# Performance work log

Measured on AMD Instinct MI355X. Metric: run time of the kernel, lower is better.

The kernel has to match this reference:

```python
import jax, jax.numpy as jnp
import numpy as np

# ---- static config (eval-mode RPN, torchvision-style FPN) ----
LEVEL_HW = [(200, 200), (100, 100), (50, 50), (25, 25), (13, 13)]
STRIDES = [4, 8, 16, 32, 64]
SIZES = [32, 64, 128, 256, 512]
A = 3                      # anchors per location (3 aspect ratios)
IMG_H, IMG_W = 800, 800
PRE_N, POST_N = 1000, 1000 # pre/post NMS top-n (testing)
NMS_TH, SCORE_TH, MIN_SIZE = 0.7, 0.0, 1e-3
BBOX_CLIP = 4.135166556742356  # log(1000/16), BoxCoder clamp
NUM_PER_LEVEL = [A * h * w for h, w in LEVEL_HW]


def _make_anchors():
    ratios = np.array([0.5, 1.0, 2.0])
    hr = np.sqrt(ratios)
    wr = 1.0 / hr
    out = []
    for (H, W), size, stride in zip(LEVEL_HW, SIZES, STRIDES):
        ws, hs = wr * size, hr * size
        base = np.stack([-ws / 2, -hs / 2, ws / 2, hs / 2], axis=1)  # [A,4]
        sx = np.arange(W) * stride
        sy = np.arange(H) * stride
        yy, xx = np.meshgrid(sy, sx, indexing='ij')
        shifts = np.stack([xx.ravel(), yy.ravel(), xx.ravel(), yy.ravel()], axis=1)
        out.append((shifts[:, None, :] + base[None, :, :]).reshape(-1, 4))
    return np.concatenate(out, 0).astype(np.float32)


def setup_inputs() -> dict:
    key = jax.random.key(0)
    ks = jax.random.split(key, 10)
    N = 4
    inp = {}
    for i, (h, w) in enumerate(LEVEL_HW):
        inp[f'obj{i}'] = jax.random.normal(ks[i], (N, A, h, w), jnp.float32)
        inp[f'delta{i}'] = 0.5 * jax.random.normal(ks[5 + i], (N, 4 * A, h, w), jnp.float32)
    inp['anchors'] = jnp.asarray(_make_anchors())
    return inp


def _decode(deltas, anchors):
    # BoxCoder.decode with weights (1,1,1,1)
    wa = anchors[:, 2] - anchors[:, 0]
    ha = anchors[:, 3] - anchors[:, 1]
    cxa = anchors[:, 0] + 0.5 * wa
    cya = anchors[:, 1] + 0.5 * ha
    dx, dy = deltas[..., 0], deltas[..., 1]
    dw = jnp.minimum(deltas[..., 2], BBOX_CLIP)
    dh = jnp.minimum(deltas[..., 3], BBOX_CLIP)
    cx = dx * wa + cxa
    cy = dy * ha + cya
    w = jnp.exp(dw) * wa
    h = jnp.exp(dh) * ha
    return jnp.stack([cx - 0.5 * w, cy - 0.5 * h, cx + 0.5 * w, cy + 0.5 * h], -1)


def _box_iou(b1, b2):
    a1 = (b1[:, 2] - b1[:, 0]) * (b1[:, 3] - b1[:, 1])
    a2 = (b2[:, 2] - b2[:, 0]) * (b2[:, 3] - b2[:, 1])
    lt = jnp.maximum(b1[:, None, :2], b2[None, :, :2])
    rb = jnp.minimum(b1[:, None, 2:], b2[None, :, 2:])
    wh = jnp.clip(rb - lt, 0.0)
    inter = wh[..., 0] * wh[..., 1]
    return inter / (a1[:, None] + a2[None, :] - inter)


def _nms_keep(iou, valid):
    # greedy NMS over score-sorted boxes; valid marks surviving pre-filters
    K = iou.shape[0]
    def body(sup, i):
        k = valid[i] & jnp.logical_not(sup[i])
        sup = sup | (k & (iou[i] > NMS_TH))
        return sup, k
    _, keeps = jax.lax.scan(body, jnp.zeros(K, bool), jnp.arange(K))
    return keeps


def _per_image(boxes, scores, lvl):
    # clip_boxes_to_image
    x1 = jnp.clip(boxes[:, 0], 0.0, IMG_W)
    y1 = jnp.clip(boxes[:, 1], 0.0, IMG_H)
    x2 = jnp.clip(boxes[:, 2], 0.0, IMG_W)
    y2 = jnp.clip(boxes[:, 3], 0.0, IMG_H)
    boxes = jnp.stack([x1, y1, x2, y2], -1)
    # remove_small_boxes + score_thresh as validity mask
    valid = (x2 - x1 >= MIN_SIZE) & (y2 - y1 >= MIN_SIZE) & (scores >= SCORE_TH)
    ms = jnp.where(valid, scores, -1.0)
    order = jnp.argsort(-ms)
    b_s, v_s, s_s, l_s = boxes[order], valid[order], scores[order], lvl[order]
    # batched_nms trick: offset boxes by level so levels never overlap
    bn = jax.lax.stop_gradient(b_s) + (l_s.astype(boxes.dtype) * (IMG_W + 1.0))[:, None]
    keep = _nms_keep(_box_iou(bn, bn), v_s)
    sel_key = jnp.where(keep, jax.lax.stop_gradient(s_s), -1.0)
    topv, topi = jax.lax.top_k(sel_key, POST_N)
    m = topv > -0.5
    fb = jnp.where(m[:, None], b_s[topi], 0.0)
    fs = jnp.where(m, s_s[topi], 0.0)
    return fb, fs


def reference(obj0, obj1, obj2, obj3, obj4, delta0, delta1, delta2, delta3, delta4, anchors):
    objs = [obj0, obj1, obj2, obj3, obj4]
    dels = [delta0, delta1, delta2, delta3, delta4]
    N = obj0.shape[0]
    # permute_and_flatten + concat (objectness C=1)
    obj = jnp.concatenate([o.transpose(0, 2, 3, 1).reshape(N, -1) for o in objs], 1)
    dl = jnp.concatenate([
        d.reshape(N, A, 4, d.shape[2], d.shape[3]).transpose(0, 3, 4, 1, 2).reshape(N, -1, 4)
        for d in dels], 1)
    proposals = _decode(dl, anchors)  # [N, total, 4]
    levels = jnp.concatenate([jnp.full((n,), i, jnp.int32) for i, n in enumerate(NUM_PER_LEVEL)])
    # per-level top-k (static split)
    idxs, off = [], 0
    for n in NUM_PER_LEVEL:
        k = min(PRE_N, n)
        _, ti = jax.lax.top_k(obj[:, off:off + n], k)
        idxs.append(ti + off)
        off += n
    top_idx = jnp.concatenate(idxs, 1)  # [N, K]
    sel_obj = jnp.take_along_axis(obj, top_idx, 1)
    sel_lvl = levels[top_idx]
    sel_box = jnp.take_along_axis(proposals, top_idx[..., None], 1)
    scores = jax.nn.sigmoid(sel_obj)
    fb, fs = jax.vmap(_per_image)(sel_box, scores, sel_lvl)
    return fb, fs
```

## Files before the change

### kernel.cpp

```cpp
#include <hip/hip_runtime.h>
#include <cstdint>
#include <cstddef>

#define NLV 5
#define NIMG 4
#define NSEL 4507
#define TSEL (NIMG * NSEL)
#define POSTN 1000
#define TCAP 8192
#define TTCAP 2048
#define NHB 16
#define PBLK 64
#define PCH 1875

__device__ const int d_W[NLV]    = {200, 100, 50, 25, 13};
__device__ const int d_NL[NLV]   = {120000, 30000, 7500, 1875, 507};
__device__ const int d_KOFF[6]   = {0, 120000, 150000, 157500, 159375, 159882};
__device__ const int d_LOFF[6]   = {0, 1000, 2000, 3000, 4000, 4507};
__device__ const int d_KL[NLV]   = {1000, 1000, 1000, 1000, 507};

struct Ptrs {
    const float* obj[NLV];
    const float* del[NLV];
    const float* anch;
};

__device__ inline unsigned int dkey_of(float f) {
    unsigned int u = __float_as_uint(f);
    unsigned int mk = (u & 0x80000000u) ? ~u : (u | 0x80000000u);
    return ~mk;
}
__device__ inline float logit_from_dkey(unsigned int dk) {
    unsigned int mk = ~dk;
    unsigned int u = (mk & 0x80000000u) ? (mk & 0x7fffffffu) : ~mk;
    return __uint_as_float(u);
}

__global__ __launch_bounds__(256) void k_hist(Ptrs P, unsigned int* hist) {
    int l = blockIdx.y, n = blockIdx.z;
    int nl_sz = d_NL[l];
    if (d_KL[l] >= nl_sz) return;
    int nlid = n * NLV + l;
    __shared__ unsigned int h[2048];
    for (int i = threadIdx.x; i < 2048; i += 256) h[i] = 0;
    __syncthreads();
    const float* ob = P.obj[l] + (size_t)n * nl_sz;
    int chunk = (nl_sz + NHB - 1) / NHB;
    int beg = blockIdx.x * chunk;
    int end = min(beg + chunk, nl_sz);
    for (int t = beg + (int)threadIdx.x; t < end; t += 256)
        atomicAdd(&h[dkey_of(ob[t]) >> 21], 1u);
    __syncthreads();
    unsigned int* out = hist + ((size_t)nlid * NHB + blockIdx.x) * 2048;
    for (int i = threadIdx.x; i < 2048; i += 256) out[i] = h[i];
}

__global__ __launch_bounds__(1024) void k_thresh(const unsigned int* hist,
                                                 unsigned int* thr,
                                                 int* scnt, int* tcnt) {
    int nlid = blockIdx.x;
    int l = nlid % NLV;
    if (threadIdx.x == 0) { scnt[nlid] = 0; tcnt[nlid] = 0; }
    if (d_KL[l] >= d_NL[l]) return;
    int tid = threadIdx.x, w = tid >> 6, lane = tid & 63;
    __shared__ unsigned int wpre[16];
    const unsigned int* hb = hist + (size_t)nlid * NHB * 2048;
    unsigned int v0 = 0, v1 = 0;
    #pragma unroll
    for (int sh = 0; sh < NHB; ++sh) {
        v0 += hb[sh * 2048 + 2 * tid];
        v1 += hb[sh * 2048 + 2 * tid + 1];
    }
    unsigned int s = v0 + v1;
    unsigned int ps = s;
    #pragma unroll
    for (int d = 1; d < 64; d <<= 1) {
        unsigned int t2 = (unsigned int)__shfl_up((int)ps, d, 64);
        if (lane >= d) ps += t2;
    }
    if (lane == 63) wpre[w] = ps;
    __syncthreads();
    unsigned int base = 0;
    #pragma unroll
    for (int ww = 0; ww < 16; ++ww) if (ww < w) base += wpre[ww];
    unsigned int incl = base + ps;
    unsigned int target = (unsigned int)d_KL[l];
    unsigned int exc0 = incl - s, inc0 = incl - v1;
    unsigned int exc1 = inc0,    inc1 = incl;
    if (exc0 < target && target <= inc0) { thr[nlid * 2] = 2 * tid;     thr[nlid * 2 + 1] = exc0; }
    if (exc1 < target && target <= inc1) { thr[nlid * 2] = 2 * tid + 1; thr[nlid * 2 + 1] = exc1; }
}

__global__ __launch_bounds__(256) void k_pick(Ptrs P, const unsigned int* thr,
                                              int* scnt, int* tcnt,
                                              int* cg, float* cl,
                                              unsigned long long* tiebuf) {
    int l = blockIdx.y, n = blockIdx.z;
    int nl_sz = d_NL[l], kl = d_KL[l];
    int nlid = n * NLV + l;
    const float* ob = P.obj[l] + (size_t)n * nl_sz;
    int cbase = n * NSEL + d_LOFF[l];
    int koff = d_KOFF[l];
    int Wl = d_W[l], HW = Wl * Wl;
    int chunk = (nl_sz + PBLK - 1) / PBLK;
    int beg = blockIdx.x * chunk;
    int end = min(beg + chunk, nl_sz);
    int tid = threadIdx.x;

    if (kl >= nl_sz) {
        for (int t = beg + tid; t < end; t += 256) {
            int a = t / HW, rem = t - a * HW;
            int p = rem * 3 + a;
            cg[cbase + p] = koff + p;
            cl[cbase + p] = ob[t];
        }
        return;
    }
    __shared__ int sp[PCH];
    __shared__ float sl[PCH];
    __shared__ unsigned long long tb[PCH];
    __shared__ int nsel, ntie, sbase, tbase;
    if (tid == 0) { nsel = 0; ntie = 0; }
    __syncthreads();

    unsigned int b0 = thr[nlid * 2];
    for (int t = beg + tid; t < end; t += 256) {
        float lg = ob[t];
        unsigned int dk = dkey_of(lg);
        unsigned int bin = dk >> 21;
        if (bin < b0) {
            int pos = atomicAdd(&nsel, 1);
            int a = t / HW, rem = t - a * HW;
            sp[pos] = rem * 3 + a;
            sl[pos] = lg;
        } else if (bin == b0) {
            int pos = atomicAdd(&ntie, 1);
            int a = t / HW, rem = t - a * HW;
            tb[pos] = ((unsigned long long)dk << 17) |
                      (unsigned long long)(unsigned int)(rem * 3 + a);
        }
    }
    __syncthreads();
    if (tid == 0) {
        sbase = atomicAdd(&scnt[nlid], nsel);
        tbase = atomicAdd(&tcnt[nlid], ntie);
    }
    __syncthreads();
    int ns = nsel, nt = ntie, sb = sbase, tbs = tbase;
    for (int i = tid; i < ns; i += 256) {
        cg[cbase + sb + i] = koff + sp[i];
        cl[cbase + sb + i] = sl[i];
    }
    for (int i = tid; i < nt; i += 256) {
        int slot = tbs + i;
        if (slot < TCAP) tiebuf[(size_t)nlid * TCAP + slot] = tb[i];
    }
}

__global__ __launch_bounds__(1024) void k_tie(const unsigned int* thr, const int* tcnt,
                                              const unsigned long long* tiebuf,
                                              int* cg, float* cl) {
    int nlid = blockIdx.x;
    int n = nlid / NLV, l = nlid % NLV;
    if (d_KL[l] >= d_NL[l]) return;
    __shared__ unsigned long long kk[TCAP];
    __shared__ unsigned long long tt[TTCAP];
    __shared__ unsigned int h2[2048];
    __shared__ unsigned int wpre[16];
    __shared__ unsigned int s_b1, s_before;
    __shared__ int ctr, ttc;
    int c = min(tcnt[nlid], TCAP);
    unsigned int cnt_lt = thr[nlid * 2 + 1];
    int need = d_KL[l] - (int)cnt_lt;
    int tid = threadIdx.x, w = tid >> 6, lane = tid & 63;
    if (tid == 0) { ctr = 0; ttc = 0; }
    h2[tid] = 0; h2[tid + 1024] = 0;
    for (int i = tid; i < c; i += 1024) kk[i] = tiebuf[(size_t)nlid * TCAP + i];
    __syncthreads();
    for (int i = tid; i < c; i += 1024)
        atomicAdd(&h2[(unsigned int)((kk[i] >> 27) & 0x7ffull)], 1u);
    __syncthreads();
    unsigned int v0 = h2[2 * tid], v1 = h2[2 * tid + 1];
    unsigned int s = v0 + v1, ps = s;
    #pragma unroll
    for (int d = 1; d < 64; d <<= 1) {
        unsigned int t2 = (unsigned int)__shfl_up((int)ps, d, 64);
        if (lane >= d) ps += t2;
    }
    if (lane == 63) wpre[w] = ps;
    __syncthreads();
    unsigned int base = 0;
    #pragma unroll
    for (int ww = 0; ww < 16; ++ww) if (ww < w) base += wpre[ww];
    unsigned int incl = base + ps;
    unsigned int target = (unsigned int)need;
    unsigned int exc0 = incl - s, inc0 = incl - v1;
    unsigned int exc1 = inc0,    inc1 = incl;
    if (exc0 < target && target <= inc0) { s_b1 = 2 * tid;     s_before = exc0; }
    if (exc1 < target && target <= inc1) { s_b1 = 2 * tid + 1; s_before = exc1; }
    __syncthreads();
    unsigned int b1 = s_b1;
    int before = (int)s_before;
    int cbase = n * NSEL + d_LOFF[l];
    int koff = d_KOFF[l];
    for (int i = tid; i < c; i += 1024) {
        unsigned long long ki = kk[i];
        unsigned int sb = (unsigned int)((ki >> 27) & 0x7ffull);
        if (sb < b1) {
            int slot = atomicAdd(&ctr, 1);
            int p = (int)(ki & 0x1ffffull);
            cg[cbase + (int)cnt_lt + slot] = koff + p;
            cl[cbase + (int)cnt_lt + slot] = logit_from_dkey((unsigned int)(ki >> 17));
        } else if (sb == b1) {
            int j = atomicAdd(&ttc, 1);
            if (j < TTCAP) tt[j] = ki;
        }
    }
    __syncthreads();
    int c2 = min(ttc, TTCAP);
    int need2 = need - before;
    for (int i = tid; i < c2; i += 1024) {
        unsigned long long ki = tt[i];
        int rank = 0;
        for (int j = 0; j < c2; ++j) rank += (tt[j] < ki) ? 1 : 0;
        if (rank < need2) {
            int p = (int)(ki & 0x1ffffull);
            cg[cbase + (int)cnt_lt + before + rank] = koff + p;
            cl[cbase + (int)cnt_lt + before + rank] = logit_from_dkey((unsigned int)(ki >> 17));
        }
    }
}

__global__ __launch_bounds__(256) void k_build(Ptrs P, const int* cg, const float* cl,
                                               unsigned long long* pkey,
                                               float4* pbox, float4* pbn, float* plog) {
#pragma clang fp contract(off)
    int t = blockIdx.x * blockDim.x + threadIdx.x;
    if (t >= NIMG * NLV * 1024) return;
    int nl = t >> 10, j = t & 1023;
    int n = nl / NLV, l = nl % NLV;
    if (j >= d_KL[l]) {
        pkey[t] = ((unsigned long long)0xFFFFFFFFu << 27) | (unsigned long long)j;
        pbox[t] = make_float4(0.f, 0.f, 0.f, 0.f);
        pbn[t]  = make_float4(0.f, 0.f, 0.f, 0.f);
        plog[t] = 0.f;
        return;
    }
    int s = n * NSEL + d_LOFF[l] + j;
    int gidx = cg[s];
    float lg = cl[s];
    int p = gidx - d_KOFF[l];
    int Wl = d_W[l];
    int HW = Wl * Wl;
    int a = p % 3, hw = p / 3;
    int h = hw / Wl, w = hw - h * Wl;
    const float* dl = P.del[l];
    size_t base = (size_t)(n * 12 + a * 4) * HW + (size_t)h * Wl + w;
    float dx = dl[base], dy = dl[base + HW];
    float dw = dl[base + 2 * (size_t)HW], dh = dl[base + 3 * (size_t)HW];
    const float* an = P.anch + 4 * (size_t)gidx;
    float ax1 = an[0], ay1 = an[1], ax2 = an[2], ay2 = an[3];
    float wa = ax2 - ax1, ha = ay2 - ay1;
    float cxa = ax1 + 0.5f * wa, cya = ay1 + 0.5f * ha;
    const float CLIPC = (float)4.135166556742356;
    dw = fminf(dw, CLIPC); dh = fminf(dh, CLIPC);
    float cx = dx * wa + cxa;
    float cy = dy * ha + cya;
    float ww = expf(dw) * wa;
    float hh = expf(dh) * ha;
    float x1 = cx - 0.5f * ww, y1 = cy - 0.5f * hh;
    float x2 = cx + 0.5f * ww, y2 = cy + 0.5f * hh;
    x1 = fminf(fmaxf(x1, 0.0f), 800.0f);
    y1 = fminf(fmaxf(y1, 0.0f), 800.0f);
    x2 = fminf(fmaxf(x2, 0.0f), 800.0f);
    y2 = fminf(fmaxf(y2, 0.0f), 800.0f);
    bool valid = (x2 - x1 >= 1e-3f) && (y2 - y1 >= 1e-3f);
    float off = (float)l * 801.0f;
    pbox[t] = make_float4(x1, y1, x2, y2);
    pbn[t]  = make_float4(x1 + off, y1 + off, x2 + off, y2 + off);
    plog[t] = lg;
    unsigned int sk = valid ? dkey_of(lg) : 0xffffffffu;
    pkey[t] = ((unsigned long long)sk << 27) |
              ((unsigned long long)(unsigned int)p << 10) | (unsigned long long)j;
}

__global__ __launch_bounds__(512) void k_sortL(const unsigned long long* pkey,
                                               const float4* pbox, const float4* pbn,
                                               const float* plog,
                                               unsigned long long* skey,
                                               float4* sboxL, float4* cboxL, float* slogL,
                                               int* ccnt) {
    __shared__ unsigned long long s[1024];
    int nl = blockIdx.x, tid = threadIdx.x;
    s[tid] = pkey[nl * 1024 + tid];
    s[tid + 512] = pkey[nl * 1024 + tid + 512];
    __syncthreads();
    for (int k = 2; k <= 1024; k <<= 1) {
        for (int j = k >> 1; j > 0; j >>= 1) {
            int i = ((tid & ~(j - 1)) << 1) | (tid & (j - 1));
            int ix = i | j;
            bool up = ((i & k) == 0);
            unsigned long long A = s[i], B = s[ix];
            if ((A > B) == up) { s[i] = B; s[ix] = A; }
            __syncthreads();
        }
    }
    for (int e = tid; e < 1024; e += 512) {
        unsigned long long key = s[e];
        int j = (int)(key & 0x3ffull);
        int src = nl * 1024 + j;
        skey[nl * 1024 + e] = key;
        sboxL[nl * 1024 + e] = pbox[src];
        cboxL[nl * 1024 + e] = pbn[src];
        slogL[nl * 1024 + e] = plog[src];
        bool v = (key >> 27) != 0xFFFFFFFFull;
        bool vn = (e < 1023) ? ((s[e + 1] >> 27) != 0xFFFFFFFFull) : false;
        if (e == 0 && !v) ccnt[nl] = 0;
        if (v && (e == 1023 || !vn)) ccnt[nl] = e + 1;
    }
}

__global__ __launch_bounds__(256) void k_mask(const float4* cboxL, const int* ccnt,
                                              unsigned long long* MT) {
#pragma clang fp contract(off)
    int n = blockIdx.z, l = blockIdx.y;
    int ci = blockIdx.x >> 4, cj = blockIdx.x & 15;
    int nl = n * NLV + l;
    int cnt = ccnt[nl];
    int nw = (cnt + 63) / 64;
    if (cj < ci || cj >= nw) return;
    __shared__ float4 bi[64], bj[64];
    int tid = threadIdx.x;
    if (tid < 64) bj[tid] = cboxL[nl * 1024 + cj * 64 + tid];
    else if (tid < 128) bi[tid - 64] = cboxL[nl * 1024 + ci * 64 + (tid - 64)];
    __syncthreads();
    int w = tid >> 6, lane = tid & 63;
    float4 B = bj[lane];
    float a2 = (B.z - B.x) * (B.w - B.y);
    unsigned long long* outp = MT + ((size_t)nl * 16 + cj) * 1024 + ci * 64;
    #pragma unroll
    for (int t = 0; t < 16; ++t) {
        int i = w * 16 + t;
        float4 A = bi[i];
        float a1 = (A.z - A.x) * (A.w - A.y);
        float ltx = fmaxf(A.x, B.x), lty = fmaxf(A.y, B.y);
        float rbx = fminf(A.z, B.z), rby = fminf(A.w, B.w);
        float wx = fmaxf(rbx - ltx, 0.f), wy = fmaxf(rby - lty, 0.f);
        float inter = wx * wy;
        float iou = inter / ((a1 + a2) - inter);
        unsigned long long word = __ballot(iou > 0.7f);
        if (lane == 0) outp[i] = word;
    }
}

__global__ __launch_bounds__(1024) void k_scan(const unsigned long long* MT,
                                               const int* ccnt,
                                               unsigned long long* keepL) {
    int l = blockIdx.x, n = blockIdx.y;
    int nl = n * NLV + l;
    int tid = threadIdx.x, w = tid >> 6, lane = tid & 63;
    __shared__ unsigned long long pendS[16];
    __shared__ unsigned long long defS[16];
    int cnt = ccnt[nl];
    int nw = (cnt + 63) / 64;

    const unsigned long long* base = MT + ((size_t)nl * 16 + w) * 1024;
    unsigned long long Dmask = 0;
    if (w < nw)
        Dmask = base[(size_t)w * 64 + lane] & ~((2ull << lane) - 1ull);
    unsigned long long rows[15];
    #pragma unroll
    for (int cc = 0; cc < 15; ++cc)
        rows[cc] = (cc < w && w < nw) ? base[(size_t)cc * 64 + lane] : 0ull;

    int nb = max(0, min(64, cnt - w * 64));
    unsigned long long pend_w = (nb == 64) ? ~0ull : ((nb > 0) ? ((1ull << nb) - 1ull) : 0ull);
    unsigned long long K_w = 0;
    if (lane == 0) pendS[w] = pend_w;
    __syncthreads();

    for (int round = 0; round < 1024; ++round) {
        unsigned long long any = 0;
        #pragma unroll
        for (int cc = 0; cc < 16; ++cc) any |= pendS[cc];
        if (!any) break;
        unsigned long long acc = ((pendS[w] >> lane) & 1ull) ? Dmask : 0ull;
        #pragma unroll
        for (int cc = 0; cc < 15; ++cc)
            if (cc < w) acc |= ((pendS[cc] >> lane) & 1ull) ? rows[cc] : 0ull;
        unsigned int vlo = (unsigned int)acc, vhi = (unsigned int)(acc >> 32);
        #pragma unroll
        for (int m = 1; m < 64; m <<= 1) {
            vlo |= (unsigned int)__shfl_xor((int)vlo, m, 64);
            vhi |= (unsigned int)__shfl_xor((int)vhi, m, 64);
        }
        unsigned long long sup = ((unsigned long long)vhi << 32) | (unsigned long long)vlo;
        unsigned long long def_w = pend_w & ~sup;
        K_w |= def_w;
        if (lane == 0) defS[w] = def_w;
        __syncthreads();
        unsigned long long acc2 = ((defS[w] >> lane) & 1ull) ? Dmask : 0ull;
        #pragma unroll
        for (int cc = 0; cc < 15; ++cc)
            if (cc < w) acc2 |= ((defS[cc] >> lane) & 1ull) ? rows[cc] : 0ull;
        unsigned int rlo = (unsigned int)acc2, rhi = (unsigned int)(acc2 >> 32);
        #pragma unroll
        for (int m = 1; m < 64; m <<= 1) {
            rlo |= (unsigned int)__shfl_xor((int)rlo, m, 64);
            rhi |= (unsigned int)__shfl_xor((int)rhi, m, 64);
        }
        unsigned long long rem = ((unsigned long long)rhi << 32) | (unsigned long long)rlo;
        pend_w &= ~def_w & ~rem;
        if (lane == 0) pendS[w] = pend_w;
        __syncthreads();
    }
    if (lane == 0) keepL[nl * 16 + w] = K_w;
}

__global__ __launch_bounds__(1024) void k_rank(const unsigned long long* skey,
                                               const unsigned long long* keepL,
                                               const int* ccnt,
                                               const float4* sboxL, const float* slogL,
                                               float* out) {
    int n = blockIdx.x, tid = threadIdx.x;
    __shared__ unsigned long long KS[NLV][1024];
    __shared__ unsigned long long kd[NLV][16];
    __shared__ int kpre[NLV][17];
    __shared__ int lcnt[NLV];
    for (int i = tid; i < POSTN; i += 1024) {
        ((float4*)out)[n * POSTN + i] = make_float4(0.f, 0.f, 0.f, 0.f);
        out[NIMG * POSTN * 4 + n * POSTN + i] = 0.f;
    }
    for (int e = tid; e < NLV * 1024; e += 1024)
        ((unsigned long long*)KS)[e] = skey[(size_t)n * NLV * 1024 + e];
    if (tid < NLV * 16) ((unsigned long long*)kd)[tid] = keepL[n * NLV * 16 + tid];
    if (tid < NLV) lcnt[tid] = ccnt[n * NLV + tid];
    __syncthreads();
    if (tid < NLV) {
        int run = 0;
        for (int q = 0; q < 16; ++q) { kpre[tid][q] = run; run += (int)__popcll(kd[tid][q]); }
        kpre[tid][16] = run;
    }
    __syncthreads();
    for (int e = tid; e < NLV * 1024; e += 1024) {
        int l = e >> 10, i = e & 1023;
        if (i >= lcnt[l]) continue;
        int q = i >> 6, b = i & 63;
        if (!((kd[l][q] >> b) & 1ull)) continue;
        int rank = kpre[l][q] + (int)__popcll(kd[l][q] & ((1ull << b) - 1ull));
        unsigned int sk = (unsigned int)(KS[l][i] >> 27);
        for (int l2 = 0; l2 < NLV; ++l2) {
            if (l2 == l) continue;
            int c2 = lcnt[l2];
            unsigned long long bound = (l2 < l)
                ? (((unsigned long long)sk + 1ull) << 27)
                : ((unsigned long long)sk << 27);
            int lo = 0, hi = c2;
            while (lo < hi) {
                int mid = (lo + hi) >> 1;
                if (KS[l2][mid] < bound) lo = mid + 1; else hi = mid;
            }
            int mq = lo >> 6, mb = lo & 63;
            rank += kpre[l2][mq] + (mb ? (int)__popcll(kd[l2][mq] & ((1ull << mb) - 1ull)) : 0);
        }
        if (rank < POSTN) {
            ((float4*)out)[n * POSTN + rank] = sboxL[(size_t)(n * NLV + l) * 1024 + i];
            float lg = slogL[(size_t)(n * NLV + l) * 1024 + i];
            out[NIMG * POSTN * 4 + n * POSTN + rank] = 1.0f / (1.0f + expf(-lg));
        }
    }
}

extern "C" void kernel_launch(void* const* d_in, const int* in_sizes, int n_in,
                              void* d_out, int out_size, void* d_ws, size_t ws_size,
                              hipStream_t stream) {
    Ptrs P;
    bool interleaved = (in_sizes[1] == 4 * in_sizes[0]);
    for (int i = 0; i < NLV; ++i) {
        if (interleaved) {
            P.obj[i] = (const float*)d_in[2 * i];
            P.del[i] = (const float*)d_in[2 * i + 1];
        } else {
            P.obj[i] = (const float*)d_in[i];
            P.del[i] = (const float*)d_in[NLV + i];
        }
    }
    P.anch = (const float*)d_in[10];

    char* w = (char*)d_ws;
    size_t off = 0;
    auto alloc = [&](size_t bytes) {
        void* p = w + off;
        off = (off + bytes + 255) & ~(size_t)255;
        return p;
    };
    const size_t NLT = (size_t)NIMG * NLV * 1024;
    unsigned int* hist = (unsigned int*)alloc((size_t)NIMG * NLV * NHB * 2048 * 4);
    int* scnt = (int*)alloc(256);
    int* tcnt = (int*)alloc(256);
    unsigned int* thr = (unsigned int*)alloc((size_t)NIMG * NLV * 2 * 4);
    unsigned long long* tiebuf = (unsigned long long*)alloc((size_t)NIMG * NLV * TCAP * 8);
    int* cg      = (int*)alloc((size_t)TSEL * 4);
    float* cl    = (float*)alloc((size_t)TSEL * 4);
    unsigned long long* pkey = (unsigned long long*)alloc(NLT * 8);
    float4* pbox = (float4*)alloc(NLT * 16);
    float4* pbn  = (float4*)alloc(NLT * 16);
    float* plog  = (float*)alloc(NLT * 4);
    unsigned long long* skey = (unsigned long long*)alloc(NLT * 8);
    float4* sboxL = (float4*)alloc(NLT * 16);
    float4* cboxL = (float4*)alloc(NLT * 16);
    float* slogL  = (float*)alloc(NLT * 4);
    int* ccnt    = (int*)alloc((size_t)NIMG * NLV * 4);
    unsigned long long* keepL = (unsigned long long*)alloc((size_t)NIMG * NLV * 16 * 8);
    unsigned long long* MT = (unsigned long long*)alloc((size_t)NIMG * NLV * 16 * 1024 * 8);
    (void)ws_size; (void)n_in;

    k_hist<<<dim3(NHB, NLV, NIMG), 256, 0, stream>>>(P, hist);
    k_thresh<<<NIMG * NLV, 1024, 0, stream>>>(hist, thr, scnt, tcnt);
    k_pick<<<dim3(PBLK, NLV, NIMG), 256, 0, stream>>>(P, thr, scnt, tcnt, cg, cl, tiebuf);
    k_tie<<<NIMG * NLV, 1024, 0, stream>>>(thr, tcnt, tiebuf, cg, cl);
    k_build<<<(NIMG * NLV * 1024) / 256, 256, 0, stream>>>(P, cg, cl, pkey, pbox, pbn, plog);
    k_sortL<<<NIMG * NLV, 512, 0, stream>>>(pkey, pbox, pbn, plog, skey, sboxL, cboxL, slogL, ccnt);
    k_mask<<<dim3(256, NLV, NIMG), 256, 0, stream>>>(cboxL, ccnt, MT);
    k_scan<<<dim3(NLV, NIMG), 1024, 0, stream>>>(MT, ccnt, keepL);
    k_rank<<<NIMG, 1024, 0, stream>>>(skey, keepL, ccnt, sboxL, slogL, (float*)d_out);
}
```

Baseline: 169.5 us.

## Fuse threshold, tie-break and box build into neighbouring kernels via last-block pattern

The threshold search now runs in the last-finishing block of k_hist, and the tie resolution now runs in the last-finishing block of k_pick. Both use an atomic arrival counter and thread fences, with the counters zeroed by a small memset. Box decoding moves from k_build into k_sortL, which keeps boxes in shared memory instead of writing and re-reading pbox, pbn, plog and pkey through global memory. This cuts three kernel launches and some global round-trips. In exchange, the serial threshold and tie work now runs on 256-thread blocks, the tie keys are read from global memory rather than shared, and the code depends on cross-block fence ordering.

Result: slower. 269.0 us (+58.7%).

```diff
diff --git a/kernel.cpp b/kernel.cpp
--- a/kernel.cpp
+++ b/kernel.cpp
@@ -36,43 +36,45 @@
     return __uint_as_float(u);
 }
 
-__global__ __launch_bounds__(256) void k_hist(Ptrs P, unsigned int* hist) {
+__global__ __launch_bounds__(256) void k_hist(Ptrs P, unsigned int* hist,
+                                              unsigned int* hcnt,
+                                              unsigned int* thr, int* scnt, int* tcnt) {
     int l = blockIdx.y, n = blockIdx.z;
     int nl_sz = d_NL[l];
     if (d_KL[l] >= nl_sz) return;
     int nlid = n * NLV + l;
+    int tid = threadIdx.x;
     __shared__ unsigned int h[2048];
-    for (int i = threadIdx.x; i < 2048; i += 256) h[i] = 0;
+    __shared__ unsigned int s_rank;
+    __shared__ unsigned int wpre[4];
+    for (int i = tid; i < 2048; i += 256) h[i] = 0;
     __syncthreads();
     const float* ob = P.obj[l] + (size_t)n * nl_sz;
     int chunk = (nl_sz + NHB - 1) / NHB;
     int beg = blockIdx.x * chunk;
     int end = min(beg + chunk, nl_sz);
-    for (int t = beg + (int)threadIdx.x; t < end; t += 256)
+    for (int t = beg + tid; t < end; t += 256)
         atomicAdd(&h[dkey_of(ob[t]) >> 21], 1u);
     __syncthreads();
     unsigned int* out = hist + ((size_t)nlid * NHB + blockIdx.x) * 2048;
-    for (int i = threadIdx.x; i < 2048; i += 256) out[i] = h[i];
-}
-
-__global__ __launch_bounds__(1024) void k_thresh(const unsigned int* hist,
-                                                 unsigned int* thr,
-                                                 int* scnt, int* tcnt) {
-    int nlid = blockIdx.x;
-    int l = nlid % NLV;
-    if (threadIdx.x == 0) { scnt[nlid] = 0; tcnt[nlid] = 0; }
-    if (d_KL[l] >= d_NL[l]) return;
-    int tid = threadIdx.x, w = tid >> 6, lane = tid & 63;
-    __shared__ unsigned int wpre[16];
+    for (int i = tid; i < 2048; i += 256) out[i] = h[i];
+    __threadfence();
+    if (tid == 0) s_rank = atomicAdd(&hcnt[nlid], 1u);
+    __syncthreads();
+    if (s_rank != NHB - 1) return;
+    __threadfence();
+
+    if (tid == 0) { scnt[nlid] = 0; tcnt[nlid] = 0; }
     const unsigned int* hb = hist + (size_t)nlid * NHB * 2048;
-    unsigned int v0 = 0, v1 = 0;
-    #pragma unroll
-    for (int sh = 0; sh < NHB; ++sh) {
-        v0 += hb[sh * 2048 + 2 * tid];
-        v1 += hb[sh * 2048 + 2 * tid + 1];
-    }
-    unsigned int s = v0 + v1;
-    unsigned int ps = s;
+    unsigned int v[8]; unsigned int s8 = 0;
+    #pragma unroll
+    for (int k = 0; k < 8; ++k) {
+        unsigned int acc = 0;
+        for (int sh = 0; sh < NHB; ++sh) acc += hb[sh * 2048 + tid * 8 + k];
+        v[k] = acc; s8 += acc;
+    }
+    int w = tid >> 6, lane = tid & 63;
+    unsigned int ps = s8;
     #pragma unroll
     for (int d = 1; d < 64; d <<= 1) {
         unsigned int t2 = (unsigned int)__shfl_up((int)ps, d, 64);
@@ -82,17 +84,21 @@
     __syncthreads();
     unsigned int base = 0;
     #pragma unroll
-    for (int ww = 0; ww < 16; ++ww) if (ww < w) base += wpre[ww];
-    unsigned int incl = base + ps;
+    for (int ww = 0; ww < 4; ++ww) if (ww < w) base += wpre[ww];
+    unsigned int run = base + ps - s8;
     unsigned int target = (unsigned int)d_KL[l];
-    unsigned int exc0 = incl - s, inc0 = incl - v1;
-    unsigned int exc1 = inc0,    inc1 = incl;
-    if (exc0 < target && target <= inc0) { thr[nlid * 2] = 2 * tid;     thr[nlid * 2 + 1] = exc0; }
-    if (exc1 < target && target <= inc1) { thr[nlid * 2] = 2 * tid + 1; thr[nlid * 2 + 1] = exc1; }
+    #pragma unroll
+    for (int k = 0; k < 8; ++k) {
+        if (run < target && target <= run + v[k]) {
+            thr[nlid * 2] = (unsigned int)(tid * 8 + k);
+            thr[nlid * 2 + 1] = run;
+        }
+        run += v[k];
+    }
 }
 
 __global__ __launch_bounds__(256) void k_pick(Ptrs P, const unsigned int* thr,
-                                              int* scnt, int* tcnt,
+                                              int* scnt, int* tcnt, unsigned int* pcnt,
                                               int* cg, float* cl,
                                               unsigned long long* tiebuf) {
     int l = blockIdx.y, n = blockIdx.z;
@@ -105,7 +111,7 @@
     int chunk = (nl_sz + PBLK - 1) / PBLK;
     int beg = blockIdx.x * chunk;
     int end = min(beg + chunk, nl_sz);
-    int tid = threadIdx.x;
+    int tid = threadIdx.x, w = tid >> 6, lane = tid & 63;
 
     if (kl >= nl_sz) {
         for (int t = beg + tid; t < end; t += 256) {
@@ -120,6 +126,7 @@
     __shared__ float sl[PCH];
     __shared__ unsigned long long tb[PCH];
     __shared__ int nsel, ntie, sbase, tbase;
+    __shared__ unsigned int s_rank;
     if (tid == 0) { nsel = 0; ntie = 0; }
     __syncthreads();
 
@@ -155,33 +162,31 @@
         int slot = tbs + i;
         if (slot < TCAP) tiebuf[(size_t)nlid * TCAP + slot] = tb[i];
     }
-}
-
-__global__ __launch_bounds__(1024) void k_tie(const unsigned int* thr, const int* tcnt,
-                                              const unsigned long long* tiebuf,
-                                              int* cg, float* cl) {
-    int nlid = blockIdx.x;
-    int n = nlid / NLV, l = nlid % NLV;
-    if (d_KL[l] >= d_NL[l]) return;
-    __shared__ unsigned long long kk[TCAP];
+    __threadfence();
+    if (tid == 0) s_rank = atomicAdd(&pcnt[nlid], 1u);
+    __syncthreads();
+    if (s_rank != PBLK - 1) return;
+    __threadfence();
+
+    __shared__ unsigned int h2[2048];
     __shared__ unsigned long long tt[TTCAP];
-    __shared__ unsigned int h2[2048];
-    __shared__ unsigned int wpre[16];
+    __shared__ unsigned int wpre[4];
     __shared__ unsigned int s_b1, s_before;
     __shared__ int ctr, ttc;
+    if (tid == 0) { ctr = 0; ttc = 0; }
+    for (int i = tid; i < 2048; i += 256) h2[i] = 0;
     int c = min(tcnt[nlid], TCAP);
     unsigned int cnt_lt = thr[nlid * 2 + 1];
-    int need = d_KL[l] - (int)cnt_lt;
-    int tid = threadIdx.x, w = tid >> 6, lane = tid & 63;
-    if (tid == 0) { ctr = 0; ttc = 0; }
-    h2[tid] = 0; h2[tid + 1024] = 0;
-    for (int i = tid; i < c; i += 1024) kk[i] = tiebuf[(size_t)nlid * TCAP + i];
-    __syncthreads();
-    for (int i = tid; i < c; i += 1024)
-        atomicAdd(&h2[(unsigned int)((kk[i] >> 27) & 0x7ffull)], 1u);
-    __syncthreads();
-    unsigned int v0 = h2[2 * tid], v1 = h2[2 * tid + 1];
-    unsigned int s = v0 + v1, ps = s;
+    int need = kl - (int)cnt_lt;
+    const unsigned long long* tbg = tiebuf + (size_t)nlid * TCAP;
+    __syncthreads();
+    for (int i = tid; i < c; i += 256)
+        atomicAdd(&h2[(unsigned int)((tbg[i] >> 27) & 0x7ffull)], 1u);
+    __syncthreads();
+    unsigned int v[8]; unsigned int s8 = 0;
+    #pragma unroll
+    for (int k = 0; k < 8; ++k) { v[k] = h2[tid * 8 + k]; s8 += v[k]; }
+    unsigned int ps = s8;
     #pragma unroll
     for (int d = 1; d < 64; d <<= 1) {
         unsigned int t2 = (unsigned int)__shfl_up((int)ps, d, 64);
@@ -191,27 +196,28 @@
     __syncthreads();
     unsigned int base = 0;
     #pragma unroll
-    for (int ww = 0; ww < 16; ++ww) if (ww < w) base += wpre[ww];
-    unsigned int incl = base + ps;
+    for (int ww = 0; ww < 4; ++ww) if (ww < w) base += wpre[ww];
+    unsigned int run = base + ps - s8;
     unsigned int target = (unsigned int)need;
-    unsigned int exc0 = incl - s, inc0 = incl - v1;
-    unsigned int exc1 = inc0,    inc1 = incl;
-    if (exc0 < target && target <= inc0) { s_b1 = 2 * tid;     s_before = exc0; }
-    if (exc1 < target && target <= inc1) { s_b1 = 2 * tid + 1; s_before = exc1; }
+    #pragma unroll
+    for (int k = 0; k < 8; ++k) {
+        if (run < target && target <= run + v[k]) {
+            s_b1 = (unsigned int)(tid * 8 + k); s_before = run;
+        }
+        run += v[k];
+    }
     __syncthreads();
     unsigned int b1 = s_b1;
     int before = (int)s_before;
-    int cbase = n * NSEL + d_LOFF[l];
-    int koff = d_KOFF[l];
-    for (int i = tid; i < c; i += 1024) {
-        unsigned long long ki = kk[i];
-        unsigned int sb = (unsigned int)((ki >> 27) & 0x7ffull);
-        if (sb < b1) {
+    for (int i = tid; i < c; i += 256) {
+        unsigned long long ki = tbg[i];
+        unsigned int sb2 = (unsigned int)((ki >> 27) & 0x7ffull);
+        if (sb2 < b1) {
             int slot = atomicAdd(&ctr, 1);
             int p = (int)(ki & 0x1ffffull);
             cg[cbase + (int)cnt_lt + slot] = koff + p;
             cl[cbase + (int)cnt_lt + slot] = logit_from_dkey((unsigned int)(ki >> 17));
-        } else if (sb == b1) {
+        } else if (sb2 == b1) {
             int j = atomicAdd(&ttc, 1);
             if (j < TTCAP) tt[j] = ki;
         }
@@ -219,7 +225,7 @@
     __syncthreads();
     int c2 = min(ttc, TTCAP);
     int need2 = need - before;
-    for (int i = tid; i < c2; i += 1024) {
+    for (int i = tid; i < c2; i += 256) {
         unsigned long long ki = tt[i];
         int rank = 0;
         for (int j = 0; j < c2; ++j) rank += (tt[j] < ki) ? 1 : 0;
@@ -231,69 +237,64 @@
     }
 }
 
-__global__ __launch_bounds__(256) void k_build(Ptrs P, const int* cg, const float* cl,
-                                               unsigned long long* pkey,
-                                               float4* pbox, float4* pbn, float* plog) {
-#pragma clang fp contract(off)
-    int t = blockIdx.x * blockDim.x + threadIdx.x;
-    if (t >= NIMG * NLV * 1024) return;
-    int nl = t >> 10, j = t & 1023;
-    int n = nl / NLV, l = nl % NLV;
-    if (j >= d_KL[l]) {
-        pkey[t] = ((unsigned long long)0xFFFFFFFFu << 27) | (unsigned long long)j;
-        pbox[t] = make_float4(0.f, 0.f, 0.f, 0.f);
-        pbn[t]  = make_float4(0.f, 0.f, 0.f, 0.f);
-        plog[t] = 0.f;
-        return;
-    }
-    int s = n * NSEL + d_LOFF[l] + j;
-    int gidx = cg[s];
-    float lg = cl[s];
-    int p = gidx - d_KOFF[l];
-    int Wl = d_W[l];
-    int HW = Wl * Wl;
-    int a = p % 3, hw = p / 3;
-    int h = hw / Wl, w = hw - h * Wl;
-    const float* dl = P.del[l];
-    size_t base = (size_t)(n * 12 + a * 4) * HW + (size_t)h * Wl + w;
-    float dx = dl[base], dy = dl[base + HW];
-    float dw = dl[base + 2 * (size_t)HW], dh = dl[base + 3 * (size_t)HW];
-    const float* an = P.anch + 4 * (size_t)gidx;
-    float ax1 = an[0], ay1 = an[1], ax2 = an[2], ay2 = an[3];
-    float wa = ax2 - ax1, ha = ay2 - ay1;
-    float cxa = ax1 + 0.5f * wa, cya = ay1 + 0.5f * ha;
-    const float CLIPC = (float)4.135166556742356;
-    dw = fminf(dw, CLIPC); dh = fminf(dh, CLIPC);
-    float cx = dx * wa + cxa;
-    float cy = dy * ha + cya;
-    float ww = expf(dw) * wa;
-    float hh = expf(dh) * ha;
-    float x1 = cx - 0.5f * ww, y1 = cy - 0.5f * hh;
-    float x2 = cx + 0.5f * ww, y2 = cy + 0.5f * hh;
-    x1 = fminf(fmaxf(x1, 0.0f), 800.0f);
-    y1 = fminf(fmaxf(y1, 0.0f), 800.0f);
-    x2 = fminf(fmaxf(x2, 0.0f), 800.0f);
-    y2 = fminf(fmaxf(y2, 0.0f), 800.0f);
-    bool valid = (x2 - x1 >= 1e-3f) && (y2 - y1 >= 1e-3f);
-    float off = (float)l * 801.0f;
-    pbox[t] = make_float4(x1, y1, x2, y2);
-    pbn[t]  = make_float4(x1 + off, y1 + off, x2 + off, y2 + off);
-    plog[t] = lg;
-    unsigned int sk = valid ? dkey_of(lg) : 0xffffffffu;
-    pkey[t] = ((unsigned long long)sk << 27) |
-              ((unsigned long long)(unsigned int)p << 10) | (unsigned long long)j;
-}
-
-__global__ __launch_bounds__(512) void k_sortL(const unsigned long long* pkey,
-                                               const float4* pbox, const float4* pbn,
-                                               const float* plog,
+__global__ __launch_bounds__(512) void k_sortL(Ptrs P, const int* cg, const float* cl,
                                                unsigned long long* skey,
                                                float4* sboxL, float4* cboxL, float* slogL,
                                                int* ccnt) {
+#pragma clang fp contract(off)
     __shared__ unsigned long long s[1024];
+    __shared__ float4 lbox[1024];
+    __shared__ float4 lbn[1024];
+    __shared__ float llog[1024];
     int nl = blockIdx.x, tid = threadIdx.x;
-    s[tid] = pkey[nl * 1024 + tid];
-    s[tid + 512] = pkey[nl * 1024 + tid + 512];
+    int n = nl / NLV, l = nl % NLV;
+    #pragma unroll
+    for (int half = 0; half < 2; ++half) {
+        int j = tid + half * 512;
+        if (j >= d_KL[l]) {
+            s[j] = ((unsigned long long)0xFFFFFFFFu << 27) | (unsigned long long)j;
+            lbox[j] = make_float4(0.f, 0.f, 0.f, 0.f);
+            lbn[j]  = make_float4(0.f, 0.f, 0.f, 0.f);
+            llog[j] = 0.f;
+            continue;
+        }
+        int src = n * NSEL + d_LOFF[l] + j;
+        int gidx = cg[src];
+        float lg = cl[src];
+        int p = gidx - d_KOFF[l];
+        int Wl = d_W[l];
+        int HW = Wl * Wl;
+        int a = p % 3, hw = p / 3;
+        int h = hw / Wl, ww2 = hw - h * Wl;
+        const float* dl = P.del[l];
+        size_t base = (size_t)(n * 12 + a * 4) * HW + (size_t)h * Wl + ww2;
+        float dx = dl[base], dy = dl[base + HW];
+        float dw = dl[base + 2 * (size_t)HW], dh = dl[base + 3 * (size_t)HW];
+        const float* an = P.anch + 4 * (size_t)gidx;
+        float ax1 = an[0], ay1 = an[1], ax2 = an[2], ay2 = an[3];
+        float wa = ax2 - ax1, ha = ay2 - ay1;
+        float cxa = ax1 + 0.5f * wa, cya = ay1 + 0.5f * ha;
+        const float CLIPC = (float)4.135166556742356;
+        dw = fminf(dw, CLIPC); dh = fminf(dh, CLIPC);
+        float cx = dx * wa + cxa;
+        float cy = dy * ha + cya;
+        float ww = expf(dw) * wa;
+        float hh = expf(dh) * ha;
+        float x1 = cx - 0.5f * ww, y1 = cy - 0.5f * hh;
+        float x2 = cx + 0.5f * ww, y2 = cy + 0.5f * hh;
+        x1 = fminf(fmaxf(x1, 0.0f), 800.0f);
+        y1 = fminf(fmaxf(y1, 0.0f), 800.0f);
+        x2 = fminf(fmaxf(x2, 0.0f), 800.0f);
+        y2 = fminf(fmaxf(y2, 0.0f), 800.0f);
+        bool valid = (x2 - x1 >= 1e-3f) && (y2 - y1 >= 1e-3f);
+        float off = (float)l * 801.0f;
+        lbox[j] = make_float4(x1, y1, x2, y2);
+        lbn[j]  = make_float4(x1 + off, y1 + off, x2 + off, y2 + off);
+        llog[j] = lg;
+        unsigned int sk = valid ? dkey_of(lg) : 0xffffffffu;
+        s[j] = ((unsigned long long)sk << 27) |
+               ((unsigned long long)(unsigned int)p << 10) | (unsigned long long)j;
+    }
     __syncthreads();
     for (int k = 2; k <= 1024; k <<= 1) {
         for (int j = k >> 1; j > 0; j >>= 1) {
@@ -308,11 +309,10 @@
     for (int e = tid; e < 1024; e += 512) {
         unsigned long long key = s[e];
         int j = (int)(key & 0x3ffull);
-        int src = nl * 1024 + j;
         skey[nl * 1024 + e] = key;
-        sboxL[nl * 1024 + e] = pbox[src];
-        cboxL[nl * 1024 + e] = pbn[src];
-        slogL[nl * 1024 + e] = plog[src];
+        sboxL[nl * 1024 + e] = lbox[j];
+        cboxL[nl * 1024 + e] = lbn[j];
+        slogL[nl * 1024 + e] = llog[j];
         bool v = (key >> 27) != 0xFFFFFFFFull;
         bool vn = (e < 1023) ? ((s[e + 1] >> 27) != 0xFFFFFFFFull) : false;
         if (e == 0 && !v) ccnt[nl] = 0;
@@ -495,6 +495,8 @@
         return p;
     };
     const size_t NLT = (size_t)NIMG * NLV * 1024;
+    unsigned int* hcnt = (unsigned int*)alloc(256);
+    unsigned int* pcnt = (unsigned int*)alloc(256);
     unsigned int* hist = (unsigned int*)alloc((size_t)NIMG * NLV * NHB * 2048 * 4);
     int* scnt = (int*)alloc(256);
     int* tcnt = (int*)alloc(256);
@@ -502,10 +504,6 @@
     unsigned long long* tiebuf = (unsigned long long*)alloc((size_t)NIMG * NLV * TCAP * 8);
     int* cg      = (int*)alloc((size_t)TSEL * 4);
     float* cl    = (float*)alloc((size_t)TSEL * 4);
-    unsigned long long* pkey = (unsigned long long*)alloc(NLT * 8);
-    float4* pbox = (float4*)alloc(NLT * 16);
-    float4* pbn  = (float4*)alloc(NLT * 16);
-    float* plog  = (float*)alloc(NLT * 4);
     unsigned long long* skey = (unsigned long long*)alloc(NLT * 8);
     float4* sboxL = (float4*)alloc(NLT * 16);
     float4* cboxL = (float4*)alloc(NLT * 16);
@@ -515,12 +513,10 @@
     unsigned long long* MT = (unsigned long long*)alloc((size_t)NIMG * NLV * 16 * 1024 * 8);
     (void)ws_size; (void)n_in;
 
-    k_hist<<<dim3(NHB, NLV, NIMG), 256, 0, stream>>>(P, hist);
-    k_thresh<<<NIMG * NLV, 1024, 0, stream>>>(hist, thr, scnt, tcnt);
-    k_pick<<<dim3(PBLK, NLV, NIMG), 256, 0, stream>>>(P, thr, scnt, tcnt, cg, cl, tiebuf);
-    k_tie<<<NIMG * NLV, 1024, 0, stream>>>(thr, tcnt, tiebuf, cg, cl);
-    k_build<<<(NIMG * NLV * 1024) / 256, 256, 0, stream>>>(P, cg, cl, pkey, pbox, pbn, plog);
-    k_sortL<<<NIMG * NLV, 512, 0, stream>>>(pkey, pbox, pbn, plog, skey, sboxL, cboxL, slogL, ccnt);
+    (void)hipMemsetAsync(hcnt, 0, 512, stream);
+    k_hist<<<dim3(NHB, NLV, NIMG), 256, 0, stream>>>(P, hist, hcnt, thr, scnt, tcnt);
+    k_pick<<<dim3(PBLK, NLV, NIMG), 256, 0, stream>>>(P, thr, scnt, tcnt, pcnt, cg, cl, tiebuf);
+    k_sortL<<<NIMG * NLV, 512, 0, stream>>>(P, cg, cl, skey, sboxL, cboxL, slogL, ccnt);
     k_mask<<<dim3(256, NLV, NIMG), 256, 0, stream>>>(cboxL, ccnt, MT);
     k_scan<<<dim3(NLV, NIMG), 1024, 0, stream>>>(MT, ccnt, keepL);
     k_rank<<<NIMG, 1024, 0, stream>>>(skey, keepL, ccnt, sboxL, slogL, (float*)d_out);
```
